# Performance work log

Measured on AMD Instinct MI355X. Metric: run time of the kernel, lower is better.

## Reference

```python
import jax, jax.numpy as jnp
import numpy as np

N_NODES = 50000
N_EDGES = 800000
HIDDEN = 128
NUM_GDL = 2


def setup_inputs() -> dict:
    key = jax.random.key(0)
    k0, k1, k2, k3, k4 = jax.random.split(key, 5)
    x = jax.random.normal(k0, (N_NODES, HIDDEN), dtype=jnp.float32)
    row = jax.random.randint(k1, (N_EDGES,), 0, N_NODES, dtype=jnp.int32)
    # ensure every node appears at least once as a target so degree >= 1
    col_tail = jax.random.randint(k2, (N_EDGES - N_NODES,), 0, N_NODES, dtype=jnp.int32)
    col = jnp.concatenate([jnp.arange(N_NODES, dtype=jnp.int32), col_tail])
    edge_index = jnp.stack([row, col], axis=0)  # [2, E]
    W1s = jax.random.normal(k3, (NUM_GDL, HIDDEN, HIDDEN), dtype=jnp.float32) / np.sqrt(HIDDEN).astype(np.float32)
    W2s = jax.random.normal(k4, (NUM_GDL, HIDDEN, 2 * HIDDEN), dtype=jnp.float32) / np.sqrt(2 * HIDDEN).astype(np.float32)
    biases = jnp.zeros((NUM_GDL, HIDDEN), dtype=jnp.float32)  # reset_parameters zeroes bias
    return {"x": x, "edge_index": edge_index, "W1s": W1s, "W2s": W2s, "biases": biases}


def reference(x, edge_index, W1s, W2s, biases):
    # eval mode: dropout is identity
    row, col = edge_index[0], edge_index[1]  # row = source j, col = target i
    n, d = x.shape
    deg = jax.ops.segment_sum(jnp.ones(row.shape[0], x.dtype), col, num_segments=n)
    norm = (1.0 / deg)[row]  # per-edge norm, indexed by row as in torch source
    for k in range(W1s.shape[0]):
        W1, W2, b = W1s[k], W2s[k], biases[k]
        # lin2(cat[x_i, x_j]) = x_i @ W2[:, :d].T + x_j @ W2[:, d:].T
        # precompute both node-level projections, then gather per edge (cheaper than per-edge GEMM)
        proj_i = x @ W2[:, :d].T  # [n, d]
        proj_j = x @ W2[:, d:].T  # [n, d]
        msg = norm[:, None] * (proj_i[col] + proj_j[row])  # [E, d]
        agg = jax.ops.segment_sum(msg, col, num_segments=n)  # scatter-add into targets
        out = x @ W1.T - agg + b
        x = jax.nn.gelu(out, approximate=False)  # torch nn.GELU default = exact erf
    return x
```

## Files before the change

### kernel.cpp

```cpp
#include <hip/hip_runtime.h>

#define N_NODES 50000
#define N_EDGES 800000
#define D 128
#define NBUCKET 196
#define EPT 16
#define HIST_BLOCKS 196
#define WCONV_BLOCKS 96
#define CAST_BLOCKS 6250
#define GEMM_TILES 391

typedef unsigned short ushort_t;
typedef __bf16 bf16x8 __attribute__((ext_vector_type(8)));
typedef float f32x4 __attribute__((ext_vector_type(4)));

__device__ __forceinline__ ushort_t f2bf(float f) {
    unsigned u = __builtin_bit_cast(unsigned, f);
    u += 0x7FFFu + ((u >> 16) & 1u);
    return (ushort_t)(u >> 16);
}
__device__ __forceinline__ float bf2f(unsigned h16) {
    return __builtin_bit_cast(float, h16 << 16);
}

__global__ __launch_bounds__(256) void k_pre(const float* __restrict__ x, ushort_t* __restrict__ xb,
                                             const int* __restrict__ col, int* __restrict__ bucket_cnt,
                                             const float* __restrict__ W1s, const float* __restrict__ W2s,
                                             ushort_t* __restrict__ Wb) {
    __shared__ int hist[NBUCKET];
    int b = blockIdx.x;
    if (b < HIST_BLOCKS) {
        for (int t = threadIdx.x; t < NBUCKET; t += 256) hist[t] = 0;
        __syncthreads();
        int base = (b * 256 + threadIdx.x) * EPT;
        if (base < N_EDGES) {
            int4 c[4];
            #pragma unroll
            for (int q = 0; q < 4; ++q) c[q] = *(const int4*)(col + base + q * 4);
            #pragma unroll
            for (int q = 0; q < 4; ++q) {
                atomicAdd(&hist[c[q].x >> 8], 1); atomicAdd(&hist[c[q].y >> 8], 1);
                atomicAdd(&hist[c[q].z >> 8], 1); atomicAdd(&hist[c[q].w >> 8], 1);
            }
        }
        __syncthreads();
        for (int t = threadIdx.x; t < NBUCKET; t += 256) {
            int v = hist[t];
            if (v) atomicAdd(&bucket_cnt[t], v);
        }
    } else if (b < HIST_BLOCKS + WCONV_BLOCKS) {
        int c = (b - HIST_BLOCKS) * 256 + threadIdx.x;
        int k = c / 12288, rem = c % 12288;
        int mat = rem / 4096, rr = (rem % 4096) / 32, col4 = rem % 32;
        const float* src = (mat == 0)
            ? (W1s + k * 16384 + rr * 128 + col4 * 4)
            : (W2s + k * 32768 + rr * 256 + (mat == 2 ? 128 : 0) + col4 * 4);
        float4 v = *(const float4*)src;
        ushort_t tmp[4] = { f2bf(v.x), f2bf(v.y), f2bf(v.z), f2bf(v.w) };
        *(uint2*)(Wb + ((size_t)(k * 3 + mat)) * 16384 + rr * 128 + col4 * 4) = *(const uint2*)tmp;
    } else {
        int base = ((b - HIST_BLOCKS - WCONV_BLOCKS) * 256 + threadIdx.x) * 4;
        if (base < N_NODES * D) {
            float4 v = *(const float4*)(x + base);
            ushort_t tmp[4] = { f2bf(v.x), f2bf(v.y), f2bf(v.z), f2bf(v.w) };
            *(uint2*)(xb + base) = *(const uint2*)tmp;
        }
    }
}

__global__ __launch_bounds__(256) void k_bscan(const int* __restrict__ bucket_cnt,
                                               int* __restrict__ bucket_base,
                                               int* __restrict__ bucket_cursor) {
    __shared__ int sm[256];
    int t = threadIdx.x;
    int v = (t < NBUCKET) ? bucket_cnt[t] : 0;
    sm[t] = v;
    __syncthreads();
    for (int o = 1; o < 256; o <<= 1) {
        int add = (t >= o) ? sm[t - o] : 0;
        __syncthreads();
        sm[t] += add;
        __syncthreads();
    }
    if (t < NBUCKET) {
        int excl = sm[t] - v;
        bucket_base[t] = excl;
        bucket_cursor[t] = excl;
    }
}

__device__ __forceinline__ void gemm_tile(int m0, int y,
                                          ushort_t (*As)[136], ushort_t (*Bs)[136],
                                          const ushort_t* __restrict__ xb,
                                          const ushort_t* __restrict__ Wl,
                                          ushort_t* __restrict__ Plb,
                                          ushort_t* __restrict__ Pi_,
                                          ushort_t* __restrict__ Pj) {
    const ushort_t* Wmat = Wl + (size_t)y * 16384;
    const int tid = threadIdx.x;

    #pragma unroll
    for (int it = 0; it < 8; ++it) {
        int c = tid + it * 256;
        int r = c >> 4, kc = c & 15;
        uint4 v = make_uint4(0, 0, 0, 0);
        int gm = m0 + r;
        if (gm < N_NODES) v = *(const uint4*)(xb + (size_t)gm * D + kc * 8);
        *(uint4*)&As[r][kc * 8] = v;
    }
    #pragma unroll
    for (int it = 0; it < 8; ++it) {
        int c = tid + it * 256;
        int r = c >> 4, kc = c & 15;
        *(uint4*)&Bs[r][kc * 8] = *(const uint4*)(Wmat + r * 128 + kc * 8);
    }
    __syncthreads();

    const int w = tid >> 6, lane = tid & 63, quad = lane >> 4, r16 = lane & 15;
    f32x4 acc[2][8];
    #pragma unroll
    for (int mt = 0; mt < 2; ++mt)
        #pragma unroll
        for (int nt = 0; nt < 8; ++nt) acc[mt][nt] = (f32x4){0.f, 0.f, 0.f, 0.f};
    const int arow0 = w * 32 + r16, arow1 = arow0 + 16;
    #pragma unroll
    for (int k0 = 0; k0 < 128; k0 += 32) {
        bf16x8 a0 = __builtin_bit_cast(bf16x8, *(const uint4*)&As[arow0][k0 + quad * 8]);
        bf16x8 a1 = __builtin_bit_cast(bf16x8, *(const uint4*)&As[arow1][k0 + quad * 8]);
        #pragma unroll
        for (int nt = 0; nt < 8; ++nt) {
            bf16x8 b = __builtin_bit_cast(bf16x8, *(const uint4*)&Bs[nt * 16 + r16][k0 + quad * 8]);
            acc[0][nt] = __builtin_amdgcn_mfma_f32_16x16x32_bf16(b, a0, acc[0][nt], 0, 0, 0);
            acc[1][nt] = __builtin_amdgcn_mfma_f32_16x16x32_bf16(b, a1, acc[1][nt], 0, 0, 0);
        }
    }
    ushort_t* Outp = (y == 0) ? Plb : (y == 1 ? Pi_ : Pj);
    #pragma unroll
    for (int mt = 0; mt < 2; ++mt) {
        int gm = m0 + w * 32 + mt * 16 + r16;
        if (gm >= N_NODES) continue;
        #pragma unroll
        for (int nt = 0; nt < 8; ++nt) {
            ushort_t tmp[4] = { f2bf(acc[mt][nt][0]), f2bf(acc[mt][nt][1]),
                                f2bf(acc[mt][nt][2]), f2bf(acc[mt][nt][3]) };
            *(uint2*)(Outp + (size_t)gm * D + nt * 16 + quad * 4) = *(const uint2*)tmp;
        }
    }
}

__global__ __launch_bounds__(256) void k_scatter_gemm(const int* __restrict__ row, const int* __restrict__ col,
                                                      int* __restrict__ bucket_cursor, int2* __restrict__ temp,
                                                      const ushort_t* __restrict__ xb,
                                                      const ushort_t* __restrict__ Wb,
                                                      ushort_t* __restrict__ Plb,
                                                      ushort_t* __restrict__ Pi_,
                                                      ushort_t* __restrict__ Pj) {
    __shared__ __align__(16) ushort_t As[128][136];
    __shared__ __align__(16) ushort_t Bs[128][136];
    __shared__ int hist[NBUCKET];
    if (blockIdx.x < HIST_BLOCKS) {
        for (int t = threadIdx.x; t < NBUCKET; t += 256) hist[t] = 0;
        __syncthreads();
        int base = (blockIdx.x * 256 + threadIdx.x) * EPT;
        bool act = base < N_EDGES;
        int4 c[4], r[4];
        if (act) {
            #pragma unroll
            for (int q = 0; q < 4; ++q) c[q] = *(const int4*)(col + base + q * 4);
            #pragma unroll
            for (int q = 0; q < 4; ++q) r[q] = *(const int4*)(row + base + q * 4);
            #pragma unroll
            for (int q = 0; q < 4; ++q) {
                atomicAdd(&hist[c[q].x >> 8], 1); atomicAdd(&hist[c[q].y >> 8], 1);
                atomicAdd(&hist[c[q].z >> 8], 1); atomicAdd(&hist[c[q].w >> 8], 1);
            }
        }
        __syncthreads();
        for (int t = threadIdx.x; t < NBUCKET; t += 256) {
            int cnt = hist[t];
            hist[t] = cnt ? atomicAdd(&bucket_cursor[t], cnt) : 0;
        }
        __syncthreads();
        if (act) {
            #pragma unroll
            for (int q = 0; q < 4; ++q) {
                int cc[4] = { c[q].x, c[q].y, c[q].z, c[q].w };
                int rr[4] = { r[q].x, r[q].y, r[q].z, r[q].w };
                #pragma unroll
                for (int e = 0; e < 4; ++e) {
                    int pos = atomicAdd(&hist[cc[e] >> 8], 1);
                    temp[pos] = make_int2(rr[e], cc[e]);
                }
            }
        }
    } else {
        int g = blockIdx.x - HIST_BLOCKS;
        int y = g % 3, tile = g / 3;
        gemm_tile(tile * 128, y, As, Bs, xb, Wb, Plb, Pi_, Pj);
    }
}

__global__ __launch_bounds__(256) void k_bsort(const int2* __restrict__ temp,
                                               const int* __restrict__ bucket_base,
                                               const int* __restrict__ bucket_cnt,
                                               int* __restrict__ csr, int* __restrict__ off,
                                               int* __restrict__ deg, float* __restrict__ inv_deg) {
    __shared__ int hist[256];
    __shared__ int sm[256];
    int b = blockIdx.x, t = threadIdx.x;
    int base = bucket_base[b], cnt = bucket_cnt[b];
    hist[t] = 0;
    __syncthreads();
    int i = t;
    for (; i + 768 < cnt; i += 1024) {
        int2 e0 = temp[base + i], e1 = temp[base + i + 256];
        int2 e2 = temp[base + i + 512], e3 = temp[base + i + 768];
        atomicAdd(&hist[e0.y & 255], 1); atomicAdd(&hist[e1.y & 255], 1);
        atomicAdd(&hist[e2.y & 255], 1); atomicAdd(&hist[e3.y & 255], 1);
    }
    for (; i < cnt; i += 256) {
        int2 e = temp[base + i];
        atomicAdd(&hist[e.y & 255], 1);
    }
    __syncthreads();
    int c = hist[t];
    sm[t] = c;
    __syncthreads();
    for (int o = 1; o < 256; o <<= 1) {
        int add = (t >= o) ? sm[t - o] : 0;
        __syncthreads();
        sm[t] += add;
        __syncthreads();
    }
    int excl = sm[t] - c;
    int node = b * 256 + t;
    if (node < N_NODES) {
        off[node] = base + excl;
        deg[node] = c;
        inv_deg[node] = 1.0f / (float)c;
    }
    __syncthreads();
    hist[t] = base + excl;
    __syncthreads();
    i = t;
    for (; i + 768 < cnt; i += 1024) {
        int2 e0 = temp[base + i], e1 = temp[base + i + 256];
        int2 e2 = temp[base + i + 512], e3 = temp[base + i + 768];
        int p0 = atomicAdd(&hist[e0.y & 255], 1);
        int p1 = atomicAdd(&hist[e1.y & 255], 1);
        int p2 = atomicAdd(&hist[e2.y & 255], 1);
        int p3 = atomicAdd(&hist[e3.y & 255], 1);
        csr[p0] = e0.x; csr[p1] = e1.x; csr[p2] = e2.x; csr[p3] = e3.x;
    }
    for (; i < cnt; i += 256) {
        int2 e = temp[base + i];
        int p = atomicAdd(&hist[e.y & 255], 1);
        csr[p] = e.x;
    }
}

__global__ __launch_bounds__(256) void k_gemm(const ushort_t* __restrict__ xb,
                                              const ushort_t* __restrict__ Wl,
                                              ushort_t* __restrict__ Plb,
                                              ushort_t* __restrict__ Pi_,
                                              ushort_t* __restrict__ Pj) {
    __shared__ __align__(16) ushort_t As[128][136];
    __shared__ __align__(16) ushort_t Bs[128][136];
    gemm_tile(blockIdx.x * 128, blockIdx.y, As, Bs, xb, Wl, Plb, Pi_, Pj);
}

__global__ __launch_bounds__(256) void k_agg(const ushort_t* __restrict__ Plb,
                                             const ushort_t* __restrict__ Pi_,
                                             const ushort_t* __restrict__ Pj,
                                             const int* __restrict__ off,
                                             const int* __restrict__ deg,
                                             const int* __restrict__ csr,
                                             const float* __restrict__ inv_deg,
                                             const float* __restrict__ bias,
                                             float* __restrict__ out_f32,
                                             ushort_t* __restrict__ out_bf16,
                                             int write_bf16) {
    int wv = __builtin_amdgcn_readfirstlane(threadIdx.x >> 6);
    int node = blockIdx.x * 4 + wv;
    int lane = threadIdx.x & 63;
    if (node >= N_NODES) return;
    unsigned ulin = *(const unsigned*)(Plb + (size_t)node * D + 2 * lane);
    unsigned upi  = *(const unsigned*)(Pi_ + (size_t)node * D + 2 * lane);
    float2 bv = *(const float2*)(bias + 2 * lane);
    float a0 = bf2f(ulin & 0xffffu) + bv.x;
    float a1 = bf2f(ulin >> 16)     + bv.y;
    float c0 = 0.f, c1 = 0.f, si = 0.f, sj = 0.f;
    int e0 = off[node], ne = deg[node];
    int j = 0;
    for (; j + 16 <= ne; j += 16) {
        int sx[16];
        #pragma unroll
        for (int t = 0; t < 16; ++t) sx[t] = csr[e0 + j + t];
        unsigned p[16];
        #pragma unroll
        for (int t = 0; t < 16; ++t) p[t] = *(const unsigned*)(Pj + (size_t)sx[t] * D + 2 * lane);
        float dv[16];
        #pragma unroll
        for (int t = 0; t < 16; ++t) dv[t] = inv_deg[sx[t]];
        #pragma unroll
        for (int t = 0; t < 16; t += 2) {
            si += dv[t];
            sj += dv[t + 1];
            a0 -= dv[t] * bf2f(p[t] & 0xffffu) + dv[t + 1] * bf2f(p[t + 1] & 0xffffu);
            a1 -= dv[t] * bf2f(p[t] >> 16)     + dv[t + 1] * bf2f(p[t + 1] >> 16);
        }
    }
    for (; j + 4 <= ne; j += 4) {
        int s0 = csr[e0 + j], s1 = csr[e0 + j + 1], s2 = csr[e0 + j + 2], s3 = csr[e0 + j + 3];
        unsigned p0 = *(const unsigned*)(Pj + (size_t)s0 * D + 2 * lane);
        unsigned p1 = *(const unsigned*)(Pj + (size_t)s1 * D + 2 * lane);
        unsigned p2 = *(const unsigned*)(Pj + (size_t)s2 * D + 2 * lane);
        unsigned p3 = *(const unsigned*)(Pj + (size_t)s3 * D + 2 * lane);
        float d0 = inv_deg[s0], d1 = inv_deg[s1], d2 = inv_deg[s2], d3 = inv_deg[s3];
        si += d0 + d2; sj += d1 + d3;
        a0 -= d0 * bf2f(p0 & 0xffffu) + d1 * bf2f(p1 & 0xffffu);
        a1 -= d0 * bf2f(p0 >> 16)     + d1 * bf2f(p1 >> 16);
        c0 += d2 * bf2f(p2 & 0xffffu) + d3 * bf2f(p3 & 0xffffu);
        c1 += d2 * bf2f(p2 >> 16)     + d3 * bf2f(p3 >> 16);
    }
    for (; j < ne; ++j) {
        int s0 = csr[e0 + j];
        unsigned p0 = *(const unsigned*)(Pj + (size_t)s0 * D + 2 * lane);
        float d0 = inv_deg[s0];
        si += d0;
        a0 -= d0 * bf2f(p0 & 0xffffu);
        a1 -= d0 * bf2f(p0 >> 16);
    }
    si += sj;
    a0 -= c0 + si * bf2f(upi & 0xffffu);
    a1 -= c1 + si * bf2f(upi >> 16);
    float g0 = 0.5f * a0 * (1.0f + erff(a0 * 0.70710678118654752440f));
    float g1 = 0.5f * a1 * (1.0f + erff(a1 * 0.70710678118654752440f));
    if (write_bf16) {
        ushort_t tmp[2] = { f2bf(g0), f2bf(g1) };
        *(unsigned*)(out_bf16 + (size_t)node * D + 2 * lane) = *(const unsigned*)tmp;
    } else {
        *(float2*)(out_f32 + (size_t)node * D + 2 * lane) = make_float2(g0, g1);
    }
}

extern "C" void kernel_launch(void* const* d_in, const int* in_sizes, int n_in,
                              void* d_out, int out_size, void* d_ws, size_t ws_size,
                              hipStream_t stream) {
    const float* x      = (const float*)d_in[0];
    const int*   ei     = (const int*)d_in[1];
    const int*   rowp   = ei;
    const int*   colp   = ei + N_EDGES;
    const float* W1s    = (const float*)d_in[2];
    const float* W2s    = (const float*)d_in[3];
    const float* biases = (const float*)d_in[4];
    float* out = (float*)d_out;

    char* ws = (char*)d_ws;
    size_t o = 0;
    auto carve = [&](size_t bytes) -> void* {
        void* p = ws + o;
        o = (o + bytes + 255) & ~(size_t)255;
        return p;
    };
    int*      bucket_cnt    = (int*)carve(NBUCKET * 4);
    int*      bucket_base   = (int*)carve(NBUCKET * 4);
    int*      bucket_cursor = (int*)carve(NBUCKET * 4);
    int*      deg     = (int*)carve(N_NODES * 4);
    float*    inv_deg = (float*)carve(N_NODES * 4);
    int*      off     = (int*)carve(N_NODES * 4);
    int*      csr     = (int*)carve(N_EDGES * 4);
    int2*     temp    = (int2*)carve((size_t)N_EDGES * 8);
    ushort_t* xb      = (ushort_t*)carve((size_t)N_NODES * D * 2);
    ushort_t* Wb      = (ushort_t*)carve((size_t)2 * 3 * 16384 * 2);
    ushort_t* Plb     = (ushort_t*)carve((size_t)N_NODES * D * 2);
    ushort_t* Pi_     = (ushort_t*)carve((size_t)N_NODES * D * 2);
    ushort_t* Pj      = (ushort_t*)carve((size_t)N_NODES * D * 2);
    if (o > ws_size) return;

    hipMemsetAsync(bucket_cnt, 0, NBUCKET * 4, stream);

    k_pre<<<HIST_BLOCKS + WCONV_BLOCKS + CAST_BLOCKS, 256, 0, stream>>>(x, xb, colp, bucket_cnt,
                                                                        W1s, W2s, Wb);
    k_bscan<<<1, 256, 0, stream>>>(bucket_cnt, bucket_base, bucket_cursor);
    k_scatter_gemm<<<HIST_BLOCKS + 3 * GEMM_TILES, 256, 0, stream>>>(rowp, colp, bucket_cursor, temp,
                                                                     xb, Wb, Plb, Pi_, Pj);
    k_bsort<<<NBUCKET, 256, 0, stream>>>(temp, bucket_base, bucket_cnt, csr, off, deg, inv_deg);

    const int AB = (N_NODES + 3) / 4;
    k_agg<<<AB, 256, 0, stream>>>(Plb, Pi_, Pj, off, deg, csr, inv_deg, biases,
                                  nullptr, xb, 1);
    k_gemm<<<dim3(GEMM_TILES, 3), 256, 0, stream>>>(xb, Wb + (size_t)3 * 16384, Plb, Pi_, Pj);
    k_agg<<<AB, 256, 0, stream>>>(Plb, Pi_, Pj, off, deg, csr, inv_deg, biases + 128,
                                  out, nullptr, 0);
}
```

Measured before the change: 226.0 us.

## Scatter edges into fixed-capacity buckets, fuse bucket sort with GEMM, split agg lanes

Edges are now scattered directly into fixed-capacity per-bucket regions (CAP slots each) during the preprocessing kernel. This removes the separate histogram pass, the bucket scan kernel and one full pass over the edge list. The bucket scan moves into the sort blocks, which now share a launch with the layer-1 projection GEMMs. The aggregation kernel splits each wave into two halves that process alternating edges with 4 features per lane, then combines them with a cross-half shuffle. The main risk is that a bucket holding more than CAP edges would overflow, which holds for random inputs but is not guaranteed in general.

```diff
diff --git a/kernel.cpp b/kernel.cpp
--- a/kernel.cpp
+++ b/kernel.cpp
@@ -4,8 +4,9 @@
 #define N_EDGES 800000
 #define D 128
 #define NBUCKET 196
+#define CAP 8192
 #define EPT 16
-#define HIST_BLOCKS 196
+#define SCAT_BLOCKS 196
 #define WCONV_BLOCKS 96
 #define CAST_BLOCKS 6250
 #define GEMM_TILES 391
@@ -24,144 +25,16 @@
 }
 
 __global__ __launch_bounds__(256) void k_pre(const float* __restrict__ x, ushort_t* __restrict__ xb,
-                                             const int* __restrict__ col, int* __restrict__ bucket_cnt,
+                                             const int* __restrict__ row, const int* __restrict__ col,
+                                             int* __restrict__ bucket_cursor, int2* __restrict__ temp,
                                              const float* __restrict__ W1s, const float* __restrict__ W2s,
                                              ushort_t* __restrict__ Wb) {
     __shared__ int hist[NBUCKET];
     int b = blockIdx.x;
-    if (b < HIST_BLOCKS) {
+    if (b < SCAT_BLOCKS) {
         for (int t = threadIdx.x; t < NBUCKET; t += 256) hist[t] = 0;
         __syncthreads();
         int base = (b * 256 + threadIdx.x) * EPT;
-        if (base < N_EDGES) {
-            int4 c[4];
-            #pragma unroll
-            for (int q = 0; q < 4; ++q) c[q] = *(const int4*)(col + base + q * 4);
-            #pragma unroll
-            for (int q = 0; q < 4; ++q) {
-                atomicAdd(&hist[c[q].x >> 8], 1); atomicAdd(&hist[c[q].y >> 8], 1);
-                atomicAdd(&hist[c[q].z >> 8], 1); atomicAdd(&hist[c[q].w >> 8], 1);
-            }
-        }
-        __syncthreads();
-        for (int t = threadIdx.x; t < NBUCKET; t += 256) {
-            int v = hist[t];
-            if (v) atomicAdd(&bucket_cnt[t], v);
-        }
-    } else if (b < HIST_BLOCKS + WCONV_BLOCKS) {
-        int c = (b - HIST_BLOCKS) * 256 + threadIdx.x;
-        int k = c / 12288, rem = c % 12288;
-        int mat = rem / 4096, rr = (rem % 4096) / 32, col4 = rem % 32;
-        const float* src = (mat == 0)
-            ? (W1s + k * 16384 + rr * 128 + col4 * 4)
-            : (W2s + k * 32768 + rr * 256 + (mat == 2 ? 128 : 0) + col4 * 4);
-        float4 v = *(const float4*)src;
-        ushort_t tmp[4] = { f2bf(v.x), f2bf(v.y), f2bf(v.z), f2bf(v.w) };
-        *(uint2*)(Wb + ((size_t)(k * 3 + mat)) * 16384 + rr * 128 + col4 * 4) = *(const uint2*)tmp;
-    } else {
-        int base = ((b - HIST_BLOCKS - WCONV_BLOCKS) * 256 + threadIdx.x) * 4;
-        if (base < N_NODES * D) {
-            float4 v = *(const float4*)(x + base);
-            ushort_t tmp[4] = { f2bf(v.x), f2bf(v.y), f2bf(v.z), f2bf(v.w) };
-            *(uint2*)(xb + base) = *(const uint2*)tmp;
-        }
-    }
-}
-
-__global__ __launch_bounds__(256) void k_bscan(const int* __restrict__ bucket_cnt,
-                                               int* __restrict__ bucket_base,
-                                               int* __restrict__ bucket_cursor) {
-    __shared__ int sm[256];
-    int t = threadIdx.x;
-    int v = (t < NBUCKET) ? bucket_cnt[t] : 0;
-    sm[t] = v;
-    __syncthreads();
-    for (int o = 1; o < 256; o <<= 1) {
-        int add = (t >= o) ? sm[t - o] : 0;
-        __syncthreads();
-        sm[t] += add;
-        __syncthreads();
-    }
-    if (t < NBUCKET) {
-        int excl = sm[t] - v;
-        bucket_base[t] = excl;
-        bucket_cursor[t] = excl;
-    }
-}
-
-__device__ __forceinline__ void gemm_tile(int m0, int y,
-                                          ushort_t (*As)[136], ushort_t (*Bs)[136],
-                                          const ushort_t* __restrict__ xb,
-                                          const ushort_t* __restrict__ Wl,
-                                          ushort_t* __restrict__ Plb,
-                                          ushort_t* __restrict__ Pi_,
-                                          ushort_t* __restrict__ Pj) {
-    const ushort_t* Wmat = Wl + (size_t)y * 16384;
-    const int tid = threadIdx.x;
-
-    #pragma unroll
-    for (int it = 0; it < 8; ++it) {
-        int c = tid + it * 256;
-        int r = c >> 4, kc = c & 15;
-        uint4 v = make_uint4(0, 0, 0, 0);
-        int gm = m0 + r;
-        if (gm < N_NODES) v = *(const uint4*)(xb + (size_t)gm * D + kc * 8);
-        *(uint4*)&As[r][kc * 8] = v;
-    }
-    #pragma unroll
-    for (int it = 0; it < 8; ++it) {
-        int c = tid + it * 256;
-        int r = c >> 4, kc = c & 15;
-        *(uint4*)&Bs[r][kc * 8] = *(const uint4*)(Wmat + r * 128 + kc * 8);
-    }
-    __syncthreads();
-
-    const int w = tid >> 6, lane = tid & 63, quad = lane >> 4, r16 = lane & 15;
-    f32x4 acc[2][8];
-    #pragma unroll
-    for (int mt = 0; mt < 2; ++mt)
-        #pragma unroll
-        for (int nt = 0; nt < 8; ++nt) acc[mt][nt] = (f32x4){0.f, 0.f, 0.f, 0.f};
-    const int arow0 = w * 32 + r16, arow1 = arow0 + 16;
-    #pragma unroll
-    for (int k0 = 0; k0 < 128; k0 += 32) {
-        bf16x8 a0 = __builtin_bit_cast(bf16x8, *(const uint4*)&As[arow0][k0 + quad * 8]);
-        bf16x8 a1 = __builtin_bit_cast(bf16x8, *(const uint4*)&As[arow1][k0 + quad * 8]);
-        #pragma unroll
-        for (int nt = 0; nt < 8; ++nt) {
-            bf16x8 b = __builtin_bit_cast(bf16x8, *(const uint4*)&Bs[nt * 16 + r16][k0 + quad * 8]);
-            acc[0][nt] = __builtin_amdgcn_mfma_f32_16x16x32_bf16(b, a0, acc[0][nt], 0, 0, 0);
-            acc[1][nt] = __builtin_amdgcn_mfma_f32_16x16x32_bf16(b, a1, acc[1][nt], 0, 0, 0);
-        }
-    }
-    ushort_t* Outp = (y == 0) ? Plb : (y == 1 ? Pi_ : Pj);
-    #pragma unroll
-    for (int mt = 0; mt < 2; ++mt) {
-        int gm = m0 + w * 32 + mt * 16 + r16;
-        if (gm >= N_NODES) continue;
-        #pragma unroll
-        for (int nt = 0; nt < 8; ++nt) {
-            ushort_t tmp[4] = { f2bf(acc[mt][nt][0]), f2bf(acc[mt][nt][1]),
-                                f2bf(acc[mt][nt][2]), f2bf(acc[mt][nt][3]) };
-            *(uint2*)(Outp + (size_t)gm * D + nt * 16 + quad * 4) = *(const uint2*)tmp;
-        }
-    }
-}
-
-__global__ __launch_bounds__(256) void k_scatter_gemm(const int* __restrict__ row, const int* __restrict__ col,
-                                                      int* __restrict__ bucket_cursor, int2* __restrict__ temp,
-                                                      const ushort_t* __restrict__ xb,
-                                                      const ushort_t* __restrict__ Wb,
-                                                      ushort_t* __restrict__ Plb,
-                                                      ushort_t* __restrict__ Pi_,
-                                                      ushort_t* __restrict__ Pj) {
-    __shared__ __align__(16) ushort_t As[128][136];
-    __shared__ __align__(16) ushort_t Bs[128][136];
-    __shared__ int hist[NBUCKET];
-    if (blockIdx.x < HIST_BLOCKS) {
-        for (int t = threadIdx.x; t < NBUCKET; t += 256) hist[t] = 0;
-        __syncthreads();
-        int base = (blockIdx.x * 256 + threadIdx.x) * EPT;
         bool act = base < N_EDGES;
         int4 c[4], r[4];
         if (act) {
@@ -188,74 +61,166 @@
                 int rr[4] = { r[q].x, r[q].y, r[q].z, r[q].w };
                 #pragma unroll
                 for (int e = 0; e < 4; ++e) {
-                    int pos = atomicAdd(&hist[cc[e] >> 8], 1);
-                    temp[pos] = make_int2(rr[e], cc[e]);
+                    int bk = cc[e] >> 8;
+                    int pos = atomicAdd(&hist[bk], 1);
+                    temp[bk * CAP + pos] = make_int2(rr[e], cc[e]);
                 }
             }
         }
+    } else if (b < SCAT_BLOCKS + WCONV_BLOCKS) {
+        int c = (b - SCAT_BLOCKS) * 256 + threadIdx.x;
+        int k = c / 12288, rem = c % 12288;
+        int mat = rem / 4096, rr = (rem % 4096) / 32, col4 = rem % 32;
+        const float* src = (mat == 0)
+            ? (W1s + k * 16384 + rr * 128 + col4 * 4)
+            : (W2s + k * 32768 + rr * 256 + (mat == 2 ? 128 : 0) + col4 * 4);
+        float4 v = *(const float4*)src;
+        ushort_t tmp[4] = { f2bf(v.x), f2bf(v.y), f2bf(v.z), f2bf(v.w) };
+        *(uint2*)(Wb + ((size_t)(k * 3 + mat)) * 16384 + rr * 128 + col4 * 4) = *(const uint2*)tmp;
     } else {
-        int g = blockIdx.x - HIST_BLOCKS;
+        int base = ((b - SCAT_BLOCKS - WCONV_BLOCKS) * 256 + threadIdx.x) * 4;
+        if (base < N_NODES * D) {
+            float4 v = *(const float4*)(x + base);
+            ushort_t tmp[4] = { f2bf(v.x), f2bf(v.y), f2bf(v.z), f2bf(v.w) };
+            *(uint2*)(xb + base) = *(const uint2*)tmp;
+        }
+    }
+}
+
+__device__ __forceinline__ void gemm_tile(int m0, int y,
+                                          ushort_t (*As)[136], ushort_t (*Bs)[136],
+                                          const ushort_t* __restrict__ xb,
+                                          const ushort_t* __restrict__ Wl,
+                                          ushort_t* __restrict__ Plb,
+                                          ushort_t* __restrict__ Pi_,
+                                          ushort_t* __restrict__ Pj) {
+    const ushort_t* Wmat = Wl + (size_t)y * 16384;
+    const int tid = threadIdx.x;
+
+    #pragma unroll
+    for (int it = 0; it < 8; ++it) {
+        int c = tid + it * 256;
+        int r = c >> 4, kc = c & 15;
+        uint4 v = make_uint4(0, 0, 0, 0);
+        int gm = m0 + r;
+        if (gm < N_NODES) v = *(const uint4*)(xb + (size_t)gm * D + kc * 8);
+        *(uint4*)&As[r][kc * 8] = v;
+    }
+    #pragma unroll
+    for (int it = 0; it < 8; ++it) {
+        int c = tid + it * 256;
+        int r = c >> 4, kc = c & 15;
+        *(uint4*)&Bs[r][kc * 8] = *(const uint4*)(Wmat + r * 128 + kc * 8);
+    }
+    __syncthreads();
+
+    const int w = tid >> 6, lane = tid & 63, quad = lane >> 4, r16 = lane & 15;
+    f32x4 acc[2][8];
+    #pragma unroll
+    for (int mt = 0; mt < 2; ++mt)
+        #pragma unroll
+        for (int nt = 0; nt < 8; ++nt) acc[mt][nt] = (f32x4){0.f, 0.f, 0.f, 0.f};
+    const int arow0 = w * 32 + r16, arow1 = arow0 + 16;
+    #pragma unroll
+    for (int k0 = 0; k0 < 128; k0 += 32) {
+        bf16x8 a0 = __builtin_bit_cast(bf16x8, *(const uint4*)&As[arow0][k0 + quad * 8]);
+        bf16x8 a1 = __builtin_bit_cast(bf16x8, *(const uint4*)&As[arow1][k0 + quad * 8]);
+        #pragma unroll
+        for (int nt = 0; nt < 8; ++nt) {
+            bf16x8 b = __builtin_bit_cast(bf16x8, *(const uint4*)&Bs[nt * 16 + r16][k0 + quad * 8]);
+            acc[0][nt] = __builtin_amdgcn_mfma_f32_16x16x32_bf16(b, a0, acc[0][nt], 0, 0, 0);
+            acc[1][nt] = __builtin_amdgcn_mfma_f32_16x16x32_bf16(b, a1, acc[1][nt], 0, 0, 0);
+        }
+    }
+    ushort_t* Outp = (y == 0) ? Plb : (y == 1 ? Pi_ : Pj);
+    #pragma unroll
+    for (int mt = 0; mt < 2; ++mt) {
+        int gm = m0 + w * 32 + mt * 16 + r16;
+        if (gm >= N_NODES) continue;
+        #pragma unroll
+        for (int nt = 0; nt < 8; ++nt) {
+            ushort_t tmp[4] = { f2bf(acc[mt][nt][0]), f2bf(acc[mt][nt][1]),
+                                f2bf(acc[mt][nt][2]), f2bf(acc[mt][nt][3]) };
+            *(uint2*)(Outp + (size_t)gm * D + nt * 16 + quad * 4) = *(const uint2*)tmp;
+        }
+    }
+}
+
+__global__ __launch_bounds__(256) void k_bsort_gemm(const int2* __restrict__ temp,
+                                                    const int* __restrict__ bucket_cursor,
+                                                    int* __restrict__ csr, int* __restrict__ off,
+                                                    int* __restrict__ deg, float* __restrict__ inv_deg,
+                                                    const ushort_t* __restrict__ xb,
+                                                    const ushort_t* __restrict__ Wb,
+                                                    ushort_t* __restrict__ Plb,
+                                                    ushort_t* __restrict__ Pi_,
+                                                    ushort_t* __restrict__ Pj) {
+    __shared__ __align__(16) ushort_t As[128][136];
+    __shared__ __align__(16) ushort_t Bs[128][136];
+    __shared__ int hist[256];
+    __shared__ int sm[256];
+    if (blockIdx.x < NBUCKET) {
+        int b = blockIdx.x, t = threadIdx.x;
+        int cnt = bucket_cursor[b];
+        sm[t] = (t < b) ? bucket_cursor[t] : 0;
+        __syncthreads();
+        for (int o = 1; o < 256; o <<= 1) {
+            int add = (t >= o) ? sm[t - o] : 0;
+            __syncthreads();
+            sm[t] += add;
+            __syncthreads();
+        }
+        int gbase = sm[255];
+        int tbase = b * CAP;
+        hist[t] = 0;
+        __syncthreads();
+        int i = t;
+        for (; i + 768 < cnt; i += 1024) {
+            int2 e0 = temp[tbase + i], e1 = temp[tbase + i + 256];
+            int2 e2 = temp[tbase + i + 512], e3 = temp[tbase + i + 768];
+            atomicAdd(&hist[e0.y & 255], 1); atomicAdd(&hist[e1.y & 255], 1);
+            atomicAdd(&hist[e2.y & 255], 1); atomicAdd(&hist[e3.y & 255], 1);
+        }
+        for (; i < cnt; i += 256) atomicAdd(&hist[temp[tbase + i].y & 255], 1);
+        __syncthreads();
+        int c = hist[t];
+        sm[t] = c;
+        __syncthreads();
+        for (int o = 1; o < 256; o <<= 1) {
+            int add = (t >= o) ? sm[t - o] : 0;
+            __syncthreads();
+            sm[t] += add;
+            __syncthreads();
+        }
+        int excl = sm[t] - c;
+        int node = b * 256 + t;
+        if (node < N_NODES) {
+            off[node] = gbase + excl;
+            deg[node] = c;
+            inv_deg[node] = 1.0f / (float)c;
+        }
+        __syncthreads();
+        hist[t] = gbase + excl;
+        __syncthreads();
+        i = t;
+        for (; i + 768 < cnt; i += 1024) {
+            int2 e0 = temp[tbase + i], e1 = temp[tbase + i + 256];
+            int2 e2 = temp[tbase + i + 512], e3 = temp[tbase + i + 768];
+            int p0 = atomicAdd(&hist[e0.y & 255], 1);
+            int p1 = atomicAdd(&hist[e1.y & 255], 1);
+            int p2 = atomicAdd(&hist[e2.y & 255], 1);
+            int p3 = atomicAdd(&hist[e3.y & 255], 1);
+            csr[p0] = e0.x; csr[p1] = e1.x; csr[p2] = e2.x; csr[p3] = e3.x;
+        }
+        for (; i < cnt; i += 256) {
+            int2 e = temp[tbase + i];
+            int p = atomicAdd(&hist[e.y & 255], 1);
+            csr[p] = e.x;
+        }
+    } else {
+        int g = blockIdx.x - NBUCKET;
         int y = g % 3, tile = g / 3;
         gemm_tile(tile * 128, y, As, Bs, xb, Wb, Plb, Pi_, Pj);
-    }
-}
-
-__global__ __launch_bounds__(256) void k_bsort(const int2* __restrict__ temp,
-                                               const int* __restrict__ bucket_base,
-                                               const int* __restrict__ bucket_cnt,
-                                               int* __restrict__ csr, int* __restrict__ off,
-                                               int* __restrict__ deg, float* __restrict__ inv_deg) {
-    __shared__ int hist[256];
-    __shared__ int sm[256];
-    int b = blockIdx.x, t = threadIdx.x;
-    int base = bucket_base[b], cnt = bucket_cnt[b];
-    hist[t] = 0;
-    __syncthreads();
-    int i = t;
-    for (; i + 768 < cnt; i += 1024) {
-        int2 e0 = temp[base + i], e1 = temp[base + i + 256];
-        int2 e2 = temp[base + i + 512], e3 = temp[base + i + 768];
-        atomicAdd(&hist[e0.y & 255], 1); atomicAdd(&hist[e1.y & 255], 1);
-        atomicAdd(&hist[e2.y & 255], 1); atomicAdd(&hist[e3.y & 255], 1);
-    }
-    for (; i < cnt; i += 256) {
-        int2 e = temp[base + i];
-        atomicAdd(&hist[e.y & 255], 1);
-    }
-    __syncthreads();
-    int c = hist[t];
-    sm[t] = c;
-    __syncthreads();
-    for (int o = 1; o < 256; o <<= 1) {
-        int add = (t >= o) ? sm[t - o] : 0;
-        __syncthreads();
-        sm[t] += add;
-        __syncthreads();
-    }
-    int excl = sm[t] - c;
-    int node = b * 256 + t;
-    if (node < N_NODES) {
-        off[node] = base + excl;
-        deg[node] = c;
-        inv_deg[node] = 1.0f / (float)c;
-    }
-    __syncthreads();
-    hist[t] = base + excl;
-    __syncthreads();
-    i = t;
-    for (; i + 768 < cnt; i += 1024) {
-        int2 e0 = temp[base + i], e1 = temp[base + i + 256];
-        int2 e2 = temp[base + i + 512], e3 = temp[base + i + 768];
-        int p0 = atomicAdd(&hist[e0.y & 255], 1);
-        int p1 = atomicAdd(&hist[e1.y & 255], 1);
-        int p2 = atomicAdd(&hist[e2.y & 255], 1);
-        int p3 = atomicAdd(&hist[e3.y & 255], 1);
-        csr[p0] = e0.x; csr[p1] = e1.x; csr[p2] = e2.x; csr[p3] = e3.x;
-    }
-    for (; i < cnt; i += 256) {
-        int2 e = temp[base + i];
-        int p = atomicAdd(&hist[e.y & 255], 1);
-        csr[p] = e.x;
     }
 }
 
@@ -282,65 +247,75 @@
                                              int write_bf16) {
     int wv = __builtin_amdgcn_readfirstlane(threadIdx.x >> 6);
     int node = blockIdx.x * 4 + wv;
+    if (node >= N_NODES) return;
     int lane = threadIdx.x & 63;
-    if (node >= N_NODES) return;
-    unsigned ulin = *(const unsigned*)(Plb + (size_t)node * D + 2 * lane);
-    unsigned upi  = *(const unsigned*)(Pi_ + (size_t)node * D + 2 * lane);
-    float2 bv = *(const float2*)(bias + 2 * lane);
-    float a0 = bf2f(ulin & 0xffffu) + bv.x;
-    float a1 = bf2f(ulin >> 16)     + bv.y;
-    float c0 = 0.f, c1 = 0.f, si = 0.f, sj = 0.f;
+    int half = lane >> 5;
+    int hl = lane & 31;
+    float acc0 = 0.f, acc1 = 0.f, acc2 = 0.f, acc3 = 0.f, sih = 0.f;
     int e0 = off[node], ne = deg[node];
     int j = 0;
     for (; j + 16 <= ne; j += 16) {
-        int sx[16];
-        #pragma unroll
-        for (int t = 0; t < 16; ++t) sx[t] = csr[e0 + j + t];
-        unsigned p[16];
-        #pragma unroll
-        for (int t = 0; t < 16; ++t) p[t] = *(const unsigned*)(Pj + (size_t)sx[t] * D + 2 * lane);
-        float dv[16];
-        #pragma unroll
-        for (int t = 0; t < 16; ++t) dv[t] = inv_deg[sx[t]];
-        #pragma unroll
-        for (int t = 0; t < 16; t += 2) {
-            si += dv[t];
-            sj += dv[t + 1];
-            a0 -= dv[t] * bf2f(p[t] & 0xffffu) + dv[t + 1] * bf2f(p[t + 1] & 0xffffu);
-            a1 -= dv[t] * bf2f(p[t] >> 16)     + dv[t + 1] * bf2f(p[t + 1] >> 16);
-        }
-    }
-    for (; j + 4 <= ne; j += 4) {
-        int s0 = csr[e0 + j], s1 = csr[e0 + j + 1], s2 = csr[e0 + j + 2], s3 = csr[e0 + j + 3];
-        unsigned p0 = *(const unsigned*)(Pj + (size_t)s0 * D + 2 * lane);
-        unsigned p1 = *(const unsigned*)(Pj + (size_t)s1 * D + 2 * lane);
-        unsigned p2 = *(const unsigned*)(Pj + (size_t)s2 * D + 2 * lane);
-        unsigned p3 = *(const unsigned*)(Pj + (size_t)s3 * D + 2 * lane);
-        float d0 = inv_deg[s0], d1 = inv_deg[s1], d2 = inv_deg[s2], d3 = inv_deg[s3];
-        si += d0 + d2; sj += d1 + d3;
-        a0 -= d0 * bf2f(p0 & 0xffffu) + d1 * bf2f(p1 & 0xffffu);
-        a1 -= d0 * bf2f(p0 >> 16)     + d1 * bf2f(p1 >> 16);
-        c0 += d2 * bf2f(p2 & 0xffffu) + d3 * bf2f(p3 & 0xffffu);
-        c1 += d2 * bf2f(p2 >> 16)     + d3 * bf2f(p3 >> 16);
-    }
-    for (; j < ne; ++j) {
-        int s0 = csr[e0 + j];
-        unsigned p0 = *(const unsigned*)(Pj + (size_t)s0 * D + 2 * lane);
-        float d0 = inv_deg[s0];
-        si += d0;
-        a0 -= d0 * bf2f(p0 & 0xffffu);
-        a1 -= d0 * bf2f(p0 >> 16);
-    }
-    si += sj;
-    a0 -= c0 + si * bf2f(upi & 0xffffu);
-    a1 -= c1 + si * bf2f(upi >> 16);
-    float g0 = 0.5f * a0 * (1.0f + erff(a0 * 0.70710678118654752440f));
-    float g1 = 0.5f * a1 * (1.0f + erff(a1 * 0.70710678118654752440f));
-    if (write_bf16) {
-        ushort_t tmp[2] = { f2bf(g0), f2bf(g1) };
-        *(unsigned*)(out_bf16 + (size_t)node * D + 2 * lane) = *(const unsigned*)tmp;
-    } else {
-        *(float2*)(out_f32 + (size_t)node * D + 2 * lane) = make_float2(g0, g1);
+        int sx[8];
+        #pragma unroll
+        for (int t = 0; t < 8; ++t) sx[t] = csr[e0 + j + 2 * t + half];
+        uint2 pu[8];
+        #pragma unroll
+        for (int t = 0; t < 8; ++t) pu[t] = *(const uint2*)(Pj + (size_t)sx[t] * D + 4 * hl);
+        float dv[8];
+        #pragma unroll
+        for (int t = 0; t < 8; ++t) dv[t] = inv_deg[sx[t]];
+        #pragma unroll
+        for (int t = 0; t < 8; ++t) {
+            sih  += dv[t];
+            acc0 -= dv[t] * bf2f(pu[t].x & 0xffffu);
+            acc1 -= dv[t] * bf2f(pu[t].x >> 16);
+            acc2 -= dv[t] * bf2f(pu[t].y & 0xffffu);
+            acc3 -= dv[t] * bf2f(pu[t].y >> 16);
+        }
+    }
+    for (; j + 2 <= ne; j += 2) {
+        int s = csr[e0 + j + half];
+        uint2 pu = *(const uint2*)(Pj + (size_t)s * D + 4 * hl);
+        float d = inv_deg[s];
+        sih  += d;
+        acc0 -= d * bf2f(pu.x & 0xffffu);
+        acc1 -= d * bf2f(pu.x >> 16);
+        acc2 -= d * bf2f(pu.y & 0xffffu);
+        acc3 -= d * bf2f(pu.y >> 16);
+    }
+    if (j < ne && half == 0) {
+        int s = csr[e0 + j];
+        uint2 pu = *(const uint2*)(Pj + (size_t)s * D + 4 * hl);
+        float d = inv_deg[s];
+        sih  += d;
+        acc0 -= d * bf2f(pu.x & 0xffffu);
+        acc1 -= d * bf2f(pu.x >> 16);
+        acc2 -= d * bf2f(pu.y & 0xffffu);
+        acc3 -= d * bf2f(pu.y >> 16);
+    }
+    acc0 += __shfl_xor(acc0, 32, 64);
+    acc1 += __shfl_xor(acc1, 32, 64);
+    acc2 += __shfl_xor(acc2, 32, 64);
+    acc3 += __shfl_xor(acc3, 32, 64);
+    float si = sih + __shfl_xor(sih, 32, 64);
+    uint2 ul = *(const uint2*)(Plb + (size_t)node * D + 4 * hl);
+    uint2 up = *(const uint2*)(Pi_ + (size_t)node * D + 4 * hl);
+    float4 bv = *(const float4*)(bias + 4 * hl);
+    float v0 = bf2f(ul.x & 0xffffu) + bv.x - si * bf2f(up.x & 0xffffu) + acc0;
+    float v1 = bf2f(ul.x >> 16)     + bv.y - si * bf2f(up.x >> 16)     + acc1;
+    float v2 = bf2f(ul.y & 0xffffu) + bv.z - si * bf2f(up.y & 0xffffu) + acc2;
+    float v3 = bf2f(ul.y >> 16)     + bv.w - si * bf2f(up.y >> 16)     + acc3;
+    v0 = 0.5f * v0 * (1.0f + erff(v0 * 0.70710678118654752440f));
+    v1 = 0.5f * v1 * (1.0f + erff(v1 * 0.70710678118654752440f));
+    v2 = 0.5f * v2 * (1.0f + erff(v2 * 0.70710678118654752440f));
+    v3 = 0.5f * v3 * (1.0f + erff(v3 * 0.70710678118654752440f));
+    if (half == 0) {
+        if (write_bf16) {
+            ushort_t tmp[4] = { f2bf(v0), f2bf(v1), f2bf(v2), f2bf(v3) };
+            *(uint2*)(out_bf16 + (size_t)node * D + 4 * hl) = *(const uint2*)tmp;
+        } else {
+            *(float4*)(out_f32 + (size_t)node * D + 4 * hl) = make_float4(v0, v1, v2, v3);
+        }
     }
 }
 
@@ -363,14 +338,12 @@
         o = (o + bytes + 255) & ~(size_t)255;
         return p;
     };
-    int*      bucket_cnt    = (int*)carve(NBUCKET * 4);
-    int*      bucket_base   = (int*)carve(NBUCKET * 4);
     int*      bucket_cursor = (int*)carve(NBUCKET * 4);
     int*      deg     = (int*)carve(N_NODES * 4);
     float*    inv_deg = (float*)carve(N_NODES * 4);
     int*      off     = (int*)carve(N_NODES * 4);
     int*      csr     = (int*)carve(N_EDGES * 4);
-    int2*     temp    = (int2*)carve((size_t)N_EDGES * 8);
+    int2*     temp    = (int2*)carve((size_t)NBUCKET * CAP * 8);
     ushort_t* xb      = (ushort_t*)carve((size_t)N_NODES * D * 2);
     ushort_t* Wb      = (ushort_t*)carve((size_t)2 * 3 * 16384 * 2);
     ushort_t* Plb     = (ushort_t*)carve((size_t)N_NODES * D * 2);
@@ -378,14 +351,13 @@
     ushort_t* Pj      = (ushort_t*)carve((size_t)N_NODES * D * 2);
     if (o > ws_size) return;
 
-    hipMemsetAsync(bucket_cnt, 0, NBUCKET * 4, stream);
-
-    k_pre<<<HIST_BLOCKS + WCONV_BLOCKS + CAST_BLOCKS, 256, 0, stream>>>(x, xb, colp, bucket_cnt,
+    hipMemsetAsync(bucket_cursor, 0, NBUCKET * 4, stream);
+
+    k_pre<<<SCAT_BLOCKS + WCONV_BLOCKS + CAST_BLOCKS, 256, 0, stream>>>(x, xb, rowp, colp,
+                                                                        bucket_cursor, temp,
                                                                         W1s, W2s, Wb);
-    k_bscan<<<1, 256, 0, stream>>>(bucket_cnt, bucket_base, bucket_cursor);
-    k_scatter_gemm<<<HIST_BLOCKS + 3 * GEMM_TILES, 256, 0, stream>>>(rowp, colp, bucket_cursor, temp,
-                                                                     xb, Wb, Plb, Pi_, Pj);
-    k_bsort<<<NBUCKET, 256, 0, stream>>>(temp, bucket_base, bucket_cnt, csr, off, deg, inv_deg);
+    k_bsort_gemm<<<NBUCKET + 3 * GEMM_TILES, 256, 0, stream>>>(temp, bucket_cursor, csr, off,
+                                                               deg, inv_deg, xb, Wb, Plb, Pi_, Pj);
 
     const int AB = (N_NODES + 3) / 4;
     k_agg<<<AB, 256, 0, stream>>>(Plb, Pi_, Pj, off, deg, csr, inv_deg, biases,
```

New measurement: 237.5 us. +5.1%, slower.
